# Optimization experiments

Hardware: AMD Instinct MI355X
Metric: run time of the kernel (lower is better)

The kernel has to match this reference:

```python
import math
import jax, jax.numpy as jnp
import numpy as np

B, S, D = 2, 2048, 4096
H, KVH = 32, 8
HD = D // H            # 128
REP = H // KVH         # 4


def setup_inputs() -> dict:
    key = jax.random.key(0)
    ks = jax.random.split(key, 7)
    scale = 1.0 / math.sqrt(D)
    return {
        "x": jax.random.normal(ks[0], (B, S, D), dtype=jnp.float32),
        "freqs_cos": jax.random.uniform(ks[1], (S, HD // 2), dtype=jnp.float32),
        "freqs_sin": jax.random.uniform(ks[2], (S, HD // 2), dtype=jnp.float32),
        "Wq": jax.random.normal(ks[3], (D, H * HD), dtype=jnp.float32) * scale,
        "Wk": jax.random.normal(ks[4], (D, KVH * HD), dtype=jnp.float32) * scale,
        "Wv": jax.random.normal(ks[5], (D, KVH * HD), dtype=jnp.float32) * scale,
        "Wo": jax.random.normal(ks[6], (H * HD, D), dtype=jnp.float32) * scale,
    }


def _rope(t, cos, sin):
    # t: [B,S,h,HD]; pairs are interleaved (reshape to (HD//2, 2) in original)
    tr = t[..., 0::2]
    ti = t[..., 1::2]
    cos = cos[None, :, None, :]  # [1,S,1,HD//2]
    sin = sin[None, :, None, :]
    out_r = tr * cos - ti * sin
    out_i = tr * sin + ti * cos
    return jnp.stack([out_r, out_i], axis=-1).reshape(t.shape)


def reference(x, freqs_cos, freqs_sin, Wq, Wk, Wv, Wo):
    b, s, _ = x.shape
    xq = (x @ Wq).reshape(b, s, H, HD)
    xk = (x @ Wk).reshape(b, s, KVH, HD)
    xv = (x @ Wv).reshape(b, s, KVH, HD)

    xq = _rope(xq, freqs_cos, freqs_sin)
    xk = _rope(xk, freqs_cos, freqs_sin)

    # GQA: repeat each kv head REP times -> [b,s,H,HD]
    xk = jnp.repeat(xk, REP, axis=2)
    xv = jnp.repeat(xv, REP, axis=2)

    q = xq.transpose(0, 2, 1, 3)  # [b,H,s,HD]
    k = xk.transpose(0, 2, 1, 3)
    v = xv.transpose(0, 2, 1, 3)

    scores = jnp.einsum('bhqd,bhkd->bhqk', q, k) / math.sqrt(HD)
    causal = jnp.tril(jnp.ones((s, s), dtype=bool))
    scores = jnp.where(causal[None, None], scores, jnp.float32(-jnp.inf))
    probs = jax.nn.softmax(scores.astype(jnp.float32), axis=-1).astype(x.dtype)

    out = jnp.einsum('bhqk,bhkd->bhqd', probs, v)
    out = out.transpose(0, 2, 1, 3).reshape(b, s, H * HD)
    return out @ Wo
```

## Files before the change

kernel.cpp:

```cpp
#include <hip/hip_runtime.h>

typedef unsigned short u16;
typedef unsigned int u32;
typedef __attribute__((ext_vector_type(8))) short bf16x8;
typedef __attribute__((ext_vector_type(8))) unsigned short u16x8;
typedef __attribute__((ext_vector_type(4))) unsigned short u16x4;
typedef __attribute__((ext_vector_type(4))) float f32x4;
typedef __attribute__((ext_vector_type(4))) unsigned int u32x4;

#define S_LEN 2048
#define NB 2
#define NH 32
#define NKVH 8
#define HD 128
#define DMODEL 4096
#define NEG_BIG (-1.0e30f)

__device__ __forceinline__ float bf2f(u16 x) {
  union { u32 u; float f; } v; v.u = ((u32)x) << 16; return v.f;
}
__device__ __forceinline__ u16 f2bf(float f) {
  union { float f; u32 u; } v; v.f = f;
  u32 r = v.u + 0x7FFFu + ((v.u >> 16) & 1u);
  return (u16)(r >> 16);
}

__device__ __forceinline__ void gload16(const void* g, void* l) {
  __builtin_amdgcn_global_load_lds(
      (const __attribute__((address_space(1))) void*)g,
      (__attribute__((address_space(3))) void*)l, 16, 0, 0);
}

__global__ __launch_bounds__(256) void convert_x(const float* __restrict__ x,
                                                 u16* __restrict__ xb)
{
  int i = blockIdx.x * 256 + threadIdx.x;
  f32x4 a = *(const f32x4*)&x[(size_t)i * 8];
  f32x4 b = *(const f32x4*)&x[(size_t)i * 8 + 4];
  u16x8 h = { f2bf(a[0]), f2bf(a[1]), f2bf(a[2]), f2bf(a[3]),
              f2bf(b[0]), f2bf(b[1]), f2bf(b[2]), f2bf(b[3]) };
  *(u16x8*)&xb[(size_t)i * 8] = h;
}

__global__ __launch_bounds__(256) void transpose_w(const float* __restrict__ W,
                                                   u16* __restrict__ out,
                                                   int N)
{
  __shared__ u16 Ls[64 * 68];
  const int t  = threadIdx.x;
  const int k0 = blockIdx.x * 64;
  const int n0 = blockIdx.y * 64;
#pragma unroll
  for (int i = 0; i < 4; ++i) {
    int kr = (t >> 4) + i * 16;
    int nc = (t & 15) * 4;
    f32x4 v = *(const f32x4*)&W[(size_t)(k0 + kr) * N + n0 + nc];
    u16x4 h = { f2bf(v[0]), f2bf(v[1]), f2bf(v[2]), f2bf(v[3]) };
    *(u16x4*)&Ls[kr * 68 + nc] = h;
  }
  __syncthreads();
#pragma unroll
  for (int i = 0; i < 2; ++i) {
    int nr = (t >> 3) + i * 32;
    int kc = (t & 7) * 8;
    u16x8 h;
#pragma unroll
    for (int j = 0; j < 8; ++j) h[j] = Ls[(kc + j) * 68 + nr];
    *(u16x8*)&out[(size_t)(n0 + nr) * 4096 + k0 + kc] = h;
  }
}

__global__ __launch_bounds__(256) void gemm_qkv(const u16* __restrict__ A,
                                                const u16* __restrict__ Bt,
                                                u16* __restrict__ Yq,
                                                u16* __restrict__ Yk,
                                                u16* __restrict__ Yv)
{
  __shared__ u16 As[128 * 32];
  __shared__ u16 Bs[128 * 32];
  const int tid  = threadIdx.x;
  const int wave = tid >> 6;
  const int lane = tid & 63;
  const int lr   = lane & 15;
  const int quad = lane >> 4;
  const int wm   = (wave >> 1) * 64;
  const int wn   = (wave & 1) * 64;
  const int bm   = blockIdx.y * 128;
  const int bn   = blockIdx.x * 128;

  const int e0  = wave * 1024;
  const int ra0 = (e0 + lane * 8) >> 5;
  const int ca0 = (lane & 3) * 8;
  const int ra1 = ra0 + 16;

  const f32x4 zero = {0.f, 0.f, 0.f, 0.f};
  f32x4 acc[4][4];
#pragma unroll
  for (int i = 0; i < 4; ++i)
#pragma unroll
    for (int j = 0; j < 4; ++j) acc[i][j] = zero;

  for (int kt = 0; kt < 4096; kt += 32) {
    __syncthreads();
    gload16(&A [(size_t)(bm + ra0) * 4096 + kt + ca0], &As[e0]);
    gload16(&A [(size_t)(bm + ra1) * 4096 + kt + ca0], &As[e0 + 512]);
    gload16(&Bt[(size_t)(bn + ra0) * 4096 + kt + ca0], &Bs[e0]);
    gload16(&Bt[(size_t)(bn + ra1) * 4096 + kt + ca0], &Bs[e0 + 512]);
    __syncthreads();

    bf16x8 af[4], bfr[4];
#pragma unroll
    for (int mt = 0; mt < 4; ++mt)
      af[mt] = *(const bf16x8*)&As[(wm + mt * 16 + lr) * 32 + quad * 8];
#pragma unroll
    for (int nt = 0; nt < 4; ++nt)
      bfr[nt] = *(const bf16x8*)&Bs[(wn + nt * 16 + lr) * 32 + quad * 8];
#pragma unroll
    for (int mt = 0; mt < 4; ++mt)
#pragma unroll
      for (int nt = 0; nt < 4; ++nt)
        acc[mt][nt] = __builtin_amdgcn_mfma_f32_16x16x32_bf16(af[mt], bfr[nt], acc[mt][nt], 0, 0, 0);
  }

  u16* dst; size_t ldc; int nbase;
  if (bn < 4096)      { dst = Yq; ldc = 4096; nbase = bn; }
  else if (bn < 5120) { dst = Yk; ldc = 1024; nbase = bn - 4096; }
  else                { dst = Yv; ldc = 1024; nbase = bn - 5120; }
#pragma unroll
  for (int mt = 0; mt < 4; ++mt)
#pragma unroll
    for (int nt = 0; nt < 4; ++nt)
#pragma unroll
      for (int r = 0; r < 4; ++r) {
        size_t m = (size_t)(bm + wm + mt * 16 + quad * 4 + r);
        size_t n = (size_t)(nbase + wn + nt * 16 + lr);
        dst[m * ldc + n] = f2bf(acc[mt][nt][r]);
      }
}

__global__ __launch_bounds__(256) void gemm_o(const u16* __restrict__ A,
                                              const u16* __restrict__ Bt,
                                              float* __restrict__ C)
{
  __shared__ u16 As[128 * 32];
  __shared__ u16 Bs[128 * 32];
  const int tid  = threadIdx.x;
  const int wave = tid >> 6;
  const int lane = tid & 63;
  const int lr   = lane & 15;
  const int quad = lane >> 4;
  const int wm   = (wave >> 1) * 64;
  const int wn   = (wave & 1) * 64;
  const int bm   = blockIdx.y * 128;
  const int bn   = blockIdx.x * 128;

  const int e0  = wave * 1024;
  const int ra0 = (e0 + lane * 8) >> 5;
  const int ca0 = (lane & 3) * 8;
  const int ra1 = ra0 + 16;

  const f32x4 zero = {0.f, 0.f, 0.f, 0.f};
  f32x4 acc[4][4];
#pragma unroll
  for (int i = 0; i < 4; ++i)
#pragma unroll
    for (int j = 0; j < 4; ++j) acc[i][j] = zero;

  for (int kt = 0; kt < 4096; kt += 32) {
    __syncthreads();
    gload16(&A [(size_t)(bm + ra0) * 4096 + kt + ca0], &As[e0]);
    gload16(&A [(size_t)(bm + ra1) * 4096 + kt + ca0], &As[e0 + 512]);
    gload16(&Bt[(size_t)(bn + ra0) * 4096 + kt + ca0], &Bs[e0]);
    gload16(&Bt[(size_t)(bn + ra1) * 4096 + kt + ca0], &Bs[e0 + 512]);
    __syncthreads();

    bf16x8 af[4], bfr[4];
#pragma unroll
    for (int mt = 0; mt < 4; ++mt)
      af[mt] = *(const bf16x8*)&As[(wm + mt * 16 + lr) * 32 + quad * 8];
#pragma unroll
    for (int nt = 0; nt < 4; ++nt)
      bfr[nt] = *(const bf16x8*)&Bs[(wn + nt * 16 + lr) * 32 + quad * 8];
#pragma unroll
    for (int mt = 0; mt < 4; ++mt)
#pragma unroll
      for (int nt = 0; nt < 4; ++nt)
        acc[mt][nt] = __builtin_amdgcn_mfma_f32_16x16x32_bf16(af[mt], bfr[nt], acc[mt][nt], 0, 0, 0);
  }

#pragma unroll
  for (int mt = 0; mt < 4; ++mt)
#pragma unroll
    for (int nt = 0; nt < 4; ++nt)
#pragma unroll
      for (int r = 0; r < 4; ++r) {
        size_t m = (size_t)(bm + wm + mt * 16 + quad * 4 + r);
        size_t n = (size_t)(bn + wn + nt * 16 + lr);
        C[m * 4096 + n] = acc[mt][nt][r];
      }
}

__global__ __launch_bounds__(256) void rope_v(u16* __restrict__ Y,
                                              const float* __restrict__ cp,
                                              const float* __restrict__ sp,
                                              int log2nh, int total)
{
  int g = blockIdx.x * 256 + threadIdx.x;
  if (g >= total) return;
  int j = (g & 15) * 4;
  int s = (g >> (4 + log2nh)) & (S_LEN - 1);
  u16x8 t = *(const u16x8*)&Y[(size_t)g * 8];
  f32x4 c  = *(const f32x4*)&cp[s * 64 + j];
  f32x4 sn = *(const f32x4*)&sp[s * 64 + j];
  u16x8 o;
#pragma unroll
  for (int p = 0; p < 4; ++p) {
    float tr = bf2f(t[2 * p]);
    float ti = bf2f(t[2 * p + 1]);
    o[2 * p]     = f2bf(tr * c[p] - ti * sn[p]);
    o[2 * p + 1] = f2bf(tr * sn[p] + ti * c[p]);
  }
  *(u16x8*)&Y[(size_t)g * 8] = o;
}

__global__ __launch_bounds__(256) void attn_kernel(const u16* Q,
                                                   const u16* __restrict__ K,
                                                   const u16* __restrict__ V,
                                                   u16* O)
{
  __shared__ u16 Ks[64 * 136];
  __shared__ u16 Vs[128 * 72];
  __shared__ u16 Ps[4 * 16 * 72];

  const int tid  = threadIdx.x;
  const int wave = tid >> 6;
  const int lane = tid & 63;
  const int lr   = lane & 15;
  const int quad = lane >> 4;

  const int b   = blockIdx.z;
  const int h   = blockIdx.y;
  const int q0  = ((int)gridDim.x - 1 - (int)blockIdx.x) * 64;
  const int kvh = h >> 2;

  const int qrow = q0 + wave * 16 + lr;
  const u16* qptr = Q + ((size_t)((b * S_LEN + qrow) * NH + h)) * HD;
  bf16x8 aq[4];
#pragma unroll
  for (int c = 0; c < 4; ++c) aq[c] = *(const bf16x8*)(qptr + c * 32 + quad * 8);

  const f32x4 zero = {0.f, 0.f, 0.f, 0.f};
  f32x4 accO[8];
#pragma unroll
  for (int nt = 0; nt < 8; ++nt) accO[nt] = zero;
  float m_run[4], l_run[4];
#pragma unroll
  for (int r = 0; r < 4; ++r) { m_run[r] = NEG_BIG; l_run[r] = 0.f; }

  const float scale = 0.08838834764831845f;
  const int myq = q0 + wave * 16 + quad * 4;

  int krow_[4], d0_[4];
#pragma unroll
  for (int i = 0; i < 4; ++i) {
    int e = (tid + i * 256) * 8;
    krow_[i] = e >> 7;
    d0_[i]   = e & 127;
  }

  u32x4 kreg[4], vreg[4];
#pragma unroll
  for (int i = 0; i < 4; ++i) {
    size_t base = ((size_t)((b * S_LEN + krow_[i]) * NKVH + kvh)) * HD + d0_[i];
    kreg[i] = *(const u32x4*)&K[base];
    vreg[i] = *(const u32x4*)&V[base];
  }

  for (int kv0 = 0; kv0 <= q0; kv0 += 64) {
    const bool diag = (kv0 == q0);
    __syncthreads();
#pragma unroll
    for (int i = 0; i < 4; ++i) {
      *(u32x4*)&Ks[krow_[i] * 136 + d0_[i]] = kreg[i];
      union { u32x4 q; u16 h[8]; } vv; vv.q = vreg[i];
      int kr2 = krow_[i] ^ (((d0_[i] >> 3) & 7) << 3);
#pragma unroll
      for (int j = 0; j < 8; ++j) Vs[(d0_[i] + j) * 72 + kr2] = vv.h[j];
    }
    __syncthreads();

    if (kv0 + 64 <= q0) {
#pragma unroll
      for (int i = 0; i < 4; ++i) {
        size_t base =
            ((size_t)((b * S_LEN + kv0 + 64 + krow_[i]) * NKVH + kvh)) * HD + d0_[i];
        kreg[i] = *(const u32x4*)&K[base];
        vreg[i] = *(const u32x4*)&V[base];
      }
    }

    f32x4 sa[4];
#pragma unroll
    for (int t = 0; t < 4; ++t) {
      f32x4 a = zero;
#pragma unroll
      for (int c = 0; c < 4; ++c) {
        bf16x8 bk = *(const bf16x8*)&Ks[(t * 16 + lr) * 136 + c * 32 + quad * 8];
        a = __builtin_amdgcn_mfma_f32_16x16x32_bf16(aq[c], bk, a, 0, 0, 0);
      }
      sa[t] = a;
    }

    float alpha[4];
#pragma unroll
    for (int r = 0; r < 4; ++r) {
      const int row = myq + r;
      float s[4];
#pragma unroll
      for (int t = 0; t < 4; ++t) {
        float v = sa[t][r] * scale;
        if (diag) v = (kv0 + t * 16 + lr <= row) ? v : NEG_BIG;
        s[t] = v;
      }
      float mx = fmaxf(fmaxf(s[0], s[1]), fmaxf(s[2], s[3]));
#pragma unroll
      for (int off = 8; off >= 1; off >>= 1) mx = fmaxf(mx, __shfl_xor(mx, off));
      float mn = fmaxf(m_run[r], mx);
      alpha[r] = __expf(m_run[r] - mn);
      m_run[r] = mn;
      float p[4], rs = 0.f;
#pragma unroll
      for (int t = 0; t < 4; ++t) { p[t] = __expf(s[t] - mn); rs += p[t]; }
#pragma unroll
      for (int off = 8; off >= 1; off >>= 1) rs += __shfl_xor(rs, off);
      l_run[r] = l_run[r] * alpha[r] + rs;
      const int q  = quad * 4 + r;
      const int sw = (q & 7) << 3;
      const int base = wave * 1152 + q * 72;
#pragma unroll
      for (int t = 0; t < 4; ++t) Ps[base + ((t * 16 + lr) ^ sw)] = f2bf(p[t]);
    }
#pragma unroll
    for (int nt = 0; nt < 8; ++nt)
#pragma unroll
      for (int r = 0; r < 4; ++r) accO[nt][r] *= alpha[r];

#pragma unroll
    for (int kt2 = 0; kt2 < 2; ++kt2) {
      bf16x8 pf = *(const bf16x8*)&Ps[wave * 1152 + lr * 72 +
                                      ((kt2 * 32 + quad * 8) ^ ((lr & 7) << 3))];
#pragma unroll
      for (int nt = 0; nt < 8; ++nt) {
        const int d = nt * 16 + lr;
        bf16x8 vf = *(const bf16x8*)&Vs[d * 72 +
                                        ((kt2 * 32 + quad * 8) ^ (((d >> 3) & 7) << 3))];
        accO[nt] = __builtin_amdgcn_mfma_f32_16x16x32_bf16(pf, vf, accO[nt], 0, 0, 0);
      }
    }
  }

  float rl[4];
#pragma unroll
  for (int r = 0; r < 4; ++r) rl[r] = 1.0f / l_run[r];
#pragma unroll
  for (int nt = 0; nt < 8; ++nt)
#pragma unroll
    for (int r = 0; r < 4; ++r) {
      size_t q = (size_t)(q0 + wave * 16 + quad * 4 + r);
      O[((size_t)b * S_LEN + q) * DMODEL + (size_t)h * HD + nt * 16 + lr] =
          f2bf(accO[nt][r] * rl[r]);
    }
}

extern "C" void kernel_launch(void* const* d_in, const int* in_sizes, int n_in,
                              void* d_out, int out_size, void* d_ws, size_t ws_size,
                              hipStream_t stream)
{
  const float* x  = (const float*)d_in[0];
  const float* cp = (const float*)d_in[1];
  const float* sp = (const float*)d_in[2];
  const float* Wq = (const float*)d_in[3];
  const float* Wk = (const float*)d_in[4];
  const float* Wv = (const float*)d_in[5];
  const float* Wo = (const float*)d_in[6];

  u16* Wt  = (u16*)d_ws;
  u16* Yq  = Wt + (size_t)25165824;
  u16* Yk  = Yq + (size_t)16777216;
  u16* Yv  = Yk + (size_t)4194304;
  u16* att = Yq;
  u16* WoT = Wt;
  u16* xb  = (u16*)d_out;

  transpose_w<<<dim3(64, 64), 256, 0, stream>>>(Wq, Wt,                    4096);
  transpose_w<<<dim3(64, 16), 256, 0, stream>>>(Wk, Wt + (size_t)4096*4096, 1024);
  transpose_w<<<dim3(64, 16), 256, 0, stream>>>(Wv, Wt + (size_t)5120*4096, 1024);
  convert_x<<<8192, 256, 0, stream>>>(x, xb);
  gemm_qkv<<<dim3(48, 32), 256, 0, stream>>>(xb, Wt, Yq, Yk, Yv);
  rope_v<<<8192, 256, 0, stream>>>(Yq, cp, sp, 5, 2097152);
  rope_v<<<2048, 256, 0, stream>>>(Yk, cp, sp, 3, 524288);
  attn_kernel<<<dim3(32, 32, 2), 256, 0, stream>>>(Yq, Yk, Yv, att);
  transpose_w<<<dim3(64, 64), 256, 0, stream>>>(Wo, WoT, 4096);
  gemm_o<<<dim3(32, 32), 256, 0, stream>>>(att, WoT, (float*)d_out);
}
```

Before: 1.052 ms.

## Double GEMM K-tile to 64 and pre-transpose V for attention

Both projection GEMMs now stage 64-wide K slices per iteration instead of 32, which halves the number of barrier pairs and global-load rounds per output tile. A new transpose_v kernel writes V in a head-major, d-by-seq layout into the reused weight workspace. The attention kernel can then store V tiles into shared memory with 16-byte vector writes instead of eight scalar scattered writes per thread. In exchange there is an extra kernel launch and a pass over V, and the GEMMs use twice the LDS per block.

```diff
diff --git a/kernel.cpp b/kernel.cpp
--- a/kernel.cpp
+++ b/kernel.cpp
@@ -70,14 +70,45 @@
   }
 }
 
+__global__ __launch_bounds__(256) void transpose_v(const u16* __restrict__ Yv,
+                                                   u16* __restrict__ Vt)
+{
+  __shared__ u16 Ls[64 * 68];
+  const int t  = threadIdx.x;
+  const int s0 = blockIdx.x * 64;
+  const int d0 = blockIdx.y * 64;
+  const int z  = blockIdx.z;
+#pragma unroll
+  for (int i = 0; i < 2; ++i) {
+    int sr = (t >> 3) + i * 32;
+    int dc = (t & 7) * 8;
+    u16x8 v = *(const u16x8*)&Yv[((size_t)(z >> 3) * S_LEN + s0 + sr) * 1024 +
+                                 (z & 7) * 128 + d0 + dc];
+    u16x4 lo = { v[0], v[1], v[2], v[3] };
+    u16x4 hi = { v[4], v[5], v[6], v[7] };
+    *(u16x4*)&Ls[sr * 68 + dc]     = lo;
+    *(u16x4*)&Ls[sr * 68 + dc + 4] = hi;
+  }
+  __syncthreads();
+#pragma unroll
+  for (int i = 0; i < 2; ++i) {
+    int dr = (t >> 3) + i * 32;
+    int sc = (t & 7) * 8;
+    u16x8 h;
+#pragma unroll
+    for (int j = 0; j < 8; ++j) h[j] = Ls[(sc + j) * 68 + dr];
+    *(u16x8*)&Vt[((size_t)z * 128 + d0 + dr) * S_LEN + s0 + sc] = h;
+  }
+}
+
 __global__ __launch_bounds__(256) void gemm_qkv(const u16* __restrict__ A,
                                                 const u16* __restrict__ Bt,
                                                 u16* __restrict__ Yq,
                                                 u16* __restrict__ Yk,
                                                 u16* __restrict__ Yv)
 {
-  __shared__ u16 As[128 * 32];
-  __shared__ u16 Bs[128 * 32];
+  __shared__ u16 As[128 * 64];
+  __shared__ u16 Bs[128 * 64];
   const int tid  = threadIdx.x;
   const int wave = tid >> 6;
   const int lane = tid & 63;
@@ -88,10 +119,8 @@
   const int bm   = blockIdx.y * 128;
   const int bn   = blockIdx.x * 128;
 
-  const int e0  = wave * 1024;
-  const int ra0 = (e0 + lane * 8) >> 5;
-  const int ca0 = (lane & 3) * 8;
-  const int ra1 = ra0 + 16;
+  const int col = (lane & 7) * 8;
+  const int r0  = wave * 32 + (lane >> 3);
 
   const f32x4 zero = {0.f, 0.f, 0.f, 0.f};
   f32x4 acc[4][4];
@@ -100,26 +129,32 @@
 #pragma unroll
     for (int j = 0; j < 4; ++j) acc[i][j] = zero;
 
-  for (int kt = 0; kt < 4096; kt += 32) {
-    __syncthreads();
-    gload16(&A [(size_t)(bm + ra0) * 4096 + kt + ca0], &As[e0]);
-    gload16(&A [(size_t)(bm + ra1) * 4096 + kt + ca0], &As[e0 + 512]);
-    gload16(&Bt[(size_t)(bn + ra0) * 4096 + kt + ca0], &Bs[e0]);
-    gload16(&Bt[(size_t)(bn + ra1) * 4096 + kt + ca0], &Bs[e0 + 512]);
-    __syncthreads();
-
-    bf16x8 af[4], bfr[4];
-#pragma unroll
-    for (int mt = 0; mt < 4; ++mt)
-      af[mt] = *(const bf16x8*)&As[(wm + mt * 16 + lr) * 32 + quad * 8];
-#pragma unroll
-    for (int nt = 0; nt < 4; ++nt)
-      bfr[nt] = *(const bf16x8*)&Bs[(wn + nt * 16 + lr) * 32 + quad * 8];
-#pragma unroll
-    for (int mt = 0; mt < 4; ++mt)
+  for (int kt = 0; kt < 4096; kt += 64) {
+    __syncthreads();
+#pragma unroll
+    for (int c = 0; c < 4; ++c) {
+      gload16(&A [(size_t)(bm + r0 + c * 8) * 4096 + kt + col],
+              &As[wave * 2048 + c * 512]);
+      gload16(&Bt[(size_t)(bn + r0 + c * 8) * 4096 + kt + col],
+              &Bs[wave * 2048 + c * 512]);
+    }
+    __syncthreads();
+
+#pragma unroll
+    for (int kk = 0; kk < 2; ++kk) {
+      bf16x8 af[4], bfr[4];
+#pragma unroll
+      for (int mt = 0; mt < 4; ++mt)
+        af[mt] = *(const bf16x8*)&As[(wm + mt * 16 + lr) * 64 + kk * 32 + quad * 8];
 #pragma unroll
       for (int nt = 0; nt < 4; ++nt)
-        acc[mt][nt] = __builtin_amdgcn_mfma_f32_16x16x32_bf16(af[mt], bfr[nt], acc[mt][nt], 0, 0, 0);
+        bfr[nt] = *(const bf16x8*)&Bs[(wn + nt * 16 + lr) * 64 + kk * 32 + quad * 8];
+#pragma unroll
+      for (int mt = 0; mt < 4; ++mt)
+#pragma unroll
+        for (int nt = 0; nt < 4; ++nt)
+          acc[mt][nt] = __builtin_amdgcn_mfma_f32_16x16x32_bf16(af[mt], bfr[nt], acc[mt][nt], 0, 0, 0);
+    }
   }
 
   u16* dst; size_t ldc; int nbase;
@@ -142,8 +177,8 @@
                                               const u16* __restrict__ Bt,
                                               float* __restrict__ C)
 {
-  __shared__ u16 As[128 * 32];
-  __shared__ u16 Bs[128 * 32];
+  __shared__ u16 As[128 * 64];
+  __shared__ u16 Bs[128 * 64];
   const int tid  = threadIdx.x;
   const int wave = tid >> 6;
   const int lane = tid & 63;
@@ -154,10 +189,8 @@
   const int bm   = blockIdx.y * 128;
   const int bn   = blockIdx.x * 128;
 
-  const int e0  = wave * 1024;
-  const int ra0 = (e0 + lane * 8) >> 5;
-  const int ca0 = (lane & 3) * 8;
-  const int ra1 = ra0 + 16;
+  const int col = (lane & 7) * 8;
+  const int r0  = wave * 32 + (lane >> 3);
 
   const f32x4 zero = {0.f, 0.f, 0.f, 0.f};
   f32x4 acc[4][4];
@@ -166,26 +199,32 @@
 #pragma unroll
     for (int j = 0; j < 4; ++j) acc[i][j] = zero;
 
-  for (int kt = 0; kt < 4096; kt += 32) {
-    __syncthreads();
-    gload16(&A [(size_t)(bm + ra0) * 4096 + kt + ca0], &As[e0]);
-    gload16(&A [(size_t)(bm + ra1) * 4096 + kt + ca0], &As[e0 + 512]);
-    gload16(&Bt[(size_t)(bn + ra0) * 4096 + kt + ca0], &Bs[e0]);
-    gload16(&Bt[(size_t)(bn + ra1) * 4096 + kt + ca0], &Bs[e0 + 512]);
-    __syncthreads();
-
-    bf16x8 af[4], bfr[4];
-#pragma unroll
-    for (int mt = 0; mt < 4; ++mt)
-      af[mt] = *(const bf16x8*)&As[(wm + mt * 16 + lr) * 32 + quad * 8];
-#pragma unroll
-    for (int nt = 0; nt < 4; ++nt)
-      bfr[nt] = *(const bf16x8*)&Bs[(wn + nt * 16 + lr) * 32 + quad * 8];
-#pragma unroll
-    for (int mt = 0; mt < 4; ++mt)
+  for (int kt = 0; kt < 4096; kt += 64) {
+    __syncthreads();
+#pragma unroll
+    for (int c = 0; c < 4; ++c) {
+      gload16(&A [(size_t)(bm + r0 + c * 8) * 4096 + kt + col],
+              &As[wave * 2048 + c * 512]);
+      gload16(&Bt[(size_t)(bn + r0 + c * 8) * 4096 + kt + col],
+              &Bs[wave * 2048 + c * 512]);
+    }
+    __syncthreads();
+
+#pragma unroll
+    for (int kk = 0; kk < 2; ++kk) {
+      bf16x8 af[4], bfr[4];
+#pragma unroll
+      for (int mt = 0; mt < 4; ++mt)
+        af[mt] = *(const bf16x8*)&As[(wm + mt * 16 + lr) * 64 + kk * 32 + quad * 8];
 #pragma unroll
       for (int nt = 0; nt < 4; ++nt)
-        acc[mt][nt] = __builtin_amdgcn_mfma_f32_16x16x32_bf16(af[mt], bfr[nt], acc[mt][nt], 0, 0, 0);
+        bfr[nt] = *(const bf16x8*)&Bs[(wn + nt * 16 + lr) * 64 + kk * 32 + quad * 8];
+#pragma unroll
+      for (int mt = 0; mt < 4; ++mt)
+#pragma unroll
+        for (int nt = 0; nt < 4; ++nt)
+          acc[mt][nt] = __builtin_amdgcn_mfma_f32_16x16x32_bf16(af[mt], bfr[nt], acc[mt][nt], 0, 0, 0);
+    }
   }
 
 #pragma unroll
@@ -260,20 +299,25 @@
   const float scale = 0.08838834764831845f;
   const int myq = q0 + wave * 16 + quad * 4;
 
-  int krow_[4], d0_[4];
+  int krow_[4], d0_[4], vd_[4], vk8_[4];
+  size_t kbase[4], vbase[4];
 #pragma unroll
   for (int i = 0; i < 4; ++i) {
     int e = (tid + i * 256) * 8;
     krow_[i] = e >> 7;
     d0_[i]   = e & 127;
+    int cch = tid + i * 256;
+    vd_[i]  = cch >> 3;
+    vk8_[i] = cch & 7;
+    kbase[i] = ((size_t)((b * S_LEN + krow_[i]) * NKVH + kvh)) * HD + d0_[i];
+    vbase[i] = ((size_t)((b * NKVH + kvh) * HD + vd_[i])) * S_LEN + vk8_[i] * 8;
   }
 
   u32x4 kreg[4], vreg[4];
 #pragma unroll
   for (int i = 0; i < 4; ++i) {
-    size_t base = ((size_t)((b * S_LEN + krow_[i]) * NKVH + kvh)) * HD + d0_[i];
-    kreg[i] = *(const u32x4*)&K[base];
-    vreg[i] = *(const u32x4*)&V[base];
+    kreg[i] = *(const u32x4*)&K[kbase[i]];
+    vreg[i] = *(const u32x4*)&V[vbase[i]];
   }
 
   for (int kv0 = 0; kv0 <= q0; kv0 += 64) {
@@ -282,20 +326,15 @@
 #pragma unroll
     for (int i = 0; i < 4; ++i) {
       *(u32x4*)&Ks[krow_[i] * 136 + d0_[i]] = kreg[i];
-      union { u32x4 q; u16 h[8]; } vv; vv.q = vreg[i];
-      int kr2 = krow_[i] ^ (((d0_[i] >> 3) & 7) << 3);
-#pragma unroll
-      for (int j = 0; j < 8; ++j) Vs[(d0_[i] + j) * 72 + kr2] = vv.h[j];
+      *(u32x4*)&Vs[vd_[i] * 72 + ((vk8_[i] * 8) ^ (((vd_[i] >> 3) & 7) << 3))] = vreg[i];
     }
     __syncthreads();
 
     if (kv0 + 64 <= q0) {
 #pragma unroll
       for (int i = 0; i < 4; ++i) {
-        size_t base =
-            ((size_t)((b * S_LEN + kv0 + 64 + krow_[i]) * NKVH + kvh)) * HD + d0_[i];
-        kreg[i] = *(const u32x4*)&K[base];
-        vreg[i] = *(const u32x4*)&V[base];
+        kreg[i] = *(const u32x4*)&K[kbase[i] + (size_t)(kv0 + 64) * (NKVH * HD)];
+        vreg[i] = *(const u32x4*)&V[vbase[i] + kv0 + 64];
       }
     }
 
@@ -390,6 +429,7 @@
   u16* Yv  = Yk + (size_t)4194304;
   u16* att = Yq;
   u16* WoT = Wt;
+  u16* Vt  = Wt;
   u16* xb  = (u16*)d_out;
 
   transpose_w<<<dim3(64, 64), 256, 0, stream>>>(Wq, Wt,                    4096);
@@ -399,7 +439,8 @@
   gemm_qkv<<<dim3(48, 32), 256, 0, stream>>>(xb, Wt, Yq, Yk, Yv);
   rope_v<<<8192, 256, 0, stream>>>(Yq, cp, sp, 5, 2097152);
   rope_v<<<2048, 256, 0, stream>>>(Yk, cp, sp, 3, 524288);
-  attn_kernel<<<dim3(32, 32, 2), 256, 0, stream>>>(Yq, Yk, Yv, att);
+  transpose_v<<<dim3(32, 2, 16), 256, 0, stream>>>(Yv, Vt);
+  attn_kernel<<<dim3(32, 32, 2), 256, 0, stream>>>(Yq, Yk, Vt, att);
   transpose_w<<<dim3(64, 64), 256, 0, stream>>>(Wo, WoT, 4096);
   gemm_o<<<dim3(32, 32), 256, 0, stream>>>(att, WoT, (float*)d_out);
 }
```

New measurement: 1.070 ms. Within noise of the previous version (+1.7%).
